# Performance work log

Hardware: AMD Instinct MI355X
Metric: run time of the kernel (lower is better)

Reference implementation:

```python
import jax, jax.numpy as jnp
import numpy as np

TARGET_RADIUS = 0.99
EPS = 1e-8


def _effective_W_h(W_h):
    """Spectral-norm constraint: 3 power iterations (no grad through u,v),
    then rescale W_h so its spectral radius is TARGET_RADIUS."""
    dim = W_h.shape[0]
    u = jax.random.normal(jax.random.key(1), (dim,), dtype=W_h.dtype)
    u = u / jnp.linalg.norm(u)
    Ws = jax.lax.stop_gradient(W_h)
    v = None
    for _ in range(3):
        v = Ws.T @ u
        v = v / (jnp.linalg.norm(v) + EPS)
        u = Ws @ v
        u = u / (jnp.linalg.norm(u) + EPS)
    sigma = jnp.abs(u @ W_h @ v)  # grad flows only through W_h here
    return W_h * (TARGET_RADIUS / (sigma + EPS))


def setup_inputs() -> dict:
    key = jax.random.key(0)
    ks = jax.random.split(key, 6)
    T, B, D = 2048, 16, 1024
    xavier = float(np.sqrt(6.0 / (D + D)))
    return {
        "x": jax.random.normal(ks[0], (T, B, D), dtype=jnp.float32),
        "h0": jnp.zeros((B, D), dtype=jnp.float32),
        "W_x": jax.random.uniform(ks[1], (D, D), jnp.float32, -xavier, xavier),
        "W_h": jax.random.uniform(ks[2], (D, D), jnp.float32, -xavier, xavier),
        "W_delta": jax.random.uniform(ks[3], (D, D), jnp.float32, -0.1 * xavier, 0.1 * xavier),
        "b": jnp.zeros((D,), dtype=jnp.float32),
        "b_delta": jnp.full((D,), -2.0, dtype=jnp.float32),
        "b_gate": jnp.zeros((D,), dtype=jnp.float32),
    }


def reference(x, h0, W_x, W_h, W_delta, b, b_delta, b_gate):
    # x: [T, B, D]; h0: [B, D]
    W_h_eff = _effective_W_h(W_h)
    # Batch the input-side GEMMs over all timesteps at once.
    delta_raw = jnp.einsum("tbd,ed->tbe", x, W_delta) + b_delta  # [T,B,D]
    cand_x = jnp.einsum("tbd,ed->tbe", x, W_x) + b               # [T,B,D]

    def step(h_prev, inputs):
        x_t, dr_t, cx_t = inputs
        delta = jax.nn.sigmoid(dr_t)
        candidate = jnp.tanh(cx_t + h_prev @ W_h_eff.T)
        h_new = (1.0 - delta) * h_prev + delta * candidate
        out_t = h_new * jax.nn.silu(h_new + x_t + b_gate)
        return h_new, (out_t, h_new)

    _, (output, hs) = jax.lax.scan(step, h0, (x, delta_raw, cand_x))
    h = jnp.concatenate([h0[None], hs], axis=0)  # [T+1, B, D]
    return output, h
```

## Files before the change

kernel.cpp:

```cpp
#include <hip/hip_runtime.h>
#include <hip/hip_fp16.h>
#include <stdint.h>

#define TT 2048
#define BB 16
#define DD 1024
static const size_t H0OFF = 33554432;

typedef _Float16 f16;
typedef _Float16 f16x2 __attribute__((ext_vector_type(2)));
typedef _Float16 f16x8 __attribute__((ext_vector_type(8)));
typedef float f32x4 __attribute__((ext_vector_type(4)));

__device__ __forceinline__ float erfinv_xla(float x) {
  float w = -log1pf(-x * x);
  float p;
  if (w < 5.0f) {
    w -= 2.5f;
    p = 2.81022636e-08f;
    p = fmaf(p, w, 3.43273939e-07f);
    p = fmaf(p, w, -3.5233877e-06f);
    p = fmaf(p, w, -4.39150654e-06f);
    p = fmaf(p, w, 0.00021858087f);
    p = fmaf(p, w, -0.00125372503f);
    p = fmaf(p, w, -0.00417768164f);
    p = fmaf(p, w, 0.246640727f);
    p = fmaf(p, w, 1.50140941f);
  } else {
    w = sqrtf(w) - 3.0f;
    p = -0.000200214257f;
    p = fmaf(p, w, 0.000100950558f);
    p = fmaf(p, w, 0.00134934322f);
    p = fmaf(p, w, -0.00367342844f);
    p = fmaf(p, w, 0.00573950773f);
    p = fmaf(p, w, -0.0076224613f);
    p = fmaf(p, w, 0.00943887047f);
    p = fmaf(p, w, 1.00167406f);
    p = fmaf(p, w, 2.83297682f);
  }
  return p * x;
}

__device__ __forceinline__ float bits_to_normal(unsigned bits) {
  unsigned fb = (bits >> 9) | 0x3f800000u;
  float f = __uint_as_float(fb) - 1.0f;
  const float lo = -0.99999994f;
  float u = f * 2.0f + lo;
  u = fmaxf(lo, u);
  return __uint_as_float(0x3fb504f3u) * erfinv_xla(u);
}

#define TF_ROUND(r) { x0 += x1; x1 = (x1 << r) | (x1 >> (32 - r)); x1 ^= x0; }

__global__ void k_u0(float* t0, float* u) {
  __shared__ float red[512];
  int i = threadIdx.x;
  unsigned ks0 = 0u, ks1 = 1u, ks2 = 0x1BD11BDAu ^ 0u ^ 1u;
  unsigned x0 = (unsigned)i + ks0;
  unsigned x1 = (unsigned)(i + 512) + ks1;
  TF_ROUND(13) TF_ROUND(15) TF_ROUND(26) TF_ROUND(6)
  x0 += ks1; x1 += ks2 + 1u;
  TF_ROUND(17) TF_ROUND(29) TF_ROUND(16) TF_ROUND(24)
  x0 += ks2; x1 += ks0 + 2u;
  TF_ROUND(13) TF_ROUND(15) TF_ROUND(26) TF_ROUND(6)
  x0 += ks0; x1 += ks1 + 3u;
  TF_ROUND(17) TF_ROUND(29) TF_ROUND(16) TF_ROUND(24)
  x0 += ks1; x1 += ks2 + 4u;
  TF_ROUND(13) TF_ROUND(15) TF_ROUND(26) TF_ROUND(6)
  x0 += ks2; x1 += ks0 + 5u;
  float z0 = bits_to_normal(x0);
  float z1 = bits_to_normal(x1);
  t0[i] = z0; t0[i + 512] = z1;
  red[i] = z0 * z0 + z1 * z1;
  __syncthreads();
  for (int s = 256; s > 0; s >>= 1) { if (i < s) red[i] += red[i + s]; __syncthreads(); }
  float inv = 1.0f / sqrtf(red[0]);
  u[i] = t0[i] * inv; u[i + 512] = t0[i + 512] * inv;
}

__global__ void k_mvT(const float* __restrict__ W, const float* __restrict__ u,
                      float* __restrict__ out) {
  int j = blockIdx.x * 256 + threadIdx.x;
  float acc = 0.f;
  for (int i = 0; i < DD; ++i) acc = fmaf(W[(size_t)i * DD + j], u[i], acc);
  out[j] = acc;
}

__global__ void k_mv(const float* __restrict__ W, const float* __restrict__ v,
                     float* __restrict__ out) {
  int gtid = blockIdx.x * 256 + threadIdx.x;
  int wave = gtid >> 6, lane = threadIdx.x & 63;
  for (int rr = 0; rr < 16; ++rr) {
    int row = wave * 16 + rr;
    float acc = 0.f;
    for (int c = 0; c < 16; ++c) {
      int col = c * 64 + lane;
      acc = fmaf(W[(size_t)row * DD + col], v[col], acc);
    }
    for (int off = 32; off > 0; off >>= 1) acc += __shfl_down(acc, off, 64);
    if (lane == 0) out[row] = acc;
  }
}

__global__ void k_norm(const float* __restrict__ src, float* __restrict__ dst, float eps) {
  __shared__ float red[1024];
  int i = threadIdx.x;
  float xv = src[i];
  red[i] = xv * xv;
  __syncthreads();
  for (int s = 512; s > 0; s >>= 1) { if (i < s) red[i] += red[i + s]; __syncthreads(); }
  float inv = 1.0f / (sqrtf(red[0]) + eps);
  dst[i] = src[i] * inv;
}

__global__ void k_sigma(const float* __restrict__ u, const float* __restrict__ wv,
                        float* __restrict__ scale) {
  __shared__ float red[1024];
  int i = threadIdx.x;
  red[i] = u[i] * wv[i];
  __syncthreads();
  for (int s = 512; s > 0; s >>= 1) { if (i < s) red[i] += red[i + s]; __syncthreads(); }
  if (i == 0) scale[0] = 0.99f / (fabsf(red[0]) + 1e-8f);
}

__global__ void k_castWh(const float* __restrict__ Wh, const float* __restrict__ scale,
                         f16* __restrict__ WhH) {
  int i = blockIdx.x * 256 + threadIdx.x;
  float s = scale[0];
  WhH[i] = (f16)(Wh[i] * s);
}

__global__ __launch_bounds__(256) void k_gemm(const float* __restrict__ X,
                                              const float* __restrict__ Wt,
                                              const float* __restrict__ bias,
                                              float* __restrict__ Cout) {
  __shared__ __align__(16) f16 Ah[128 * 64];
  __shared__ __align__(16) f16 Bh[128 * 64];
  int m0 = blockIdx.x * 128, n0 = blockIdx.y * 128;
  int tid = threadIdx.x, lane = tid & 63, w = tid >> 6;
  int wm = w & 1, wn = w >> 1;
  int srow = tid >> 3, scol = (tid & 7) * 8;
  f32x4 acc[4][4];
#pragma unroll
  for (int i = 0; i < 4; ++i)
#pragma unroll
    for (int j = 0; j < 4; ++j) acc[i][j] = (f32x4){0.f, 0.f, 0.f, 0.f};

  for (int kt = 0; kt < 16; ++kt) {
    int k0 = kt * 64;
#pragma unroll
    for (int c = 0; c < 4; ++c) {
      int row = c * 32 + srow;
      const float4* sa = (const float4*)(X + (size_t)(m0 + row) * DD + k0 + scol);
      float4 a0 = sa[0], a1 = sa[1];
      f16x8 hv;
      hv[0] = (f16)a0.x; hv[1] = (f16)a0.y; hv[2] = (f16)a0.z; hv[3] = (f16)a0.w;
      hv[4] = (f16)a1.x; hv[5] = (f16)a1.y; hv[6] = (f16)a1.z; hv[7] = (f16)a1.w;
      *(f16x8*)&Ah[row * 64 + scol] = hv;
      const float4* sb = (const float4*)(Wt + (size_t)(n0 + row) * DD + k0 + scol);
      float4 b0 = sb[0], b1 = sb[1];
      f16x8 hw;
      hw[0] = (f16)b0.x; hw[1] = (f16)b0.y; hw[2] = (f16)b0.z; hw[3] = (f16)b0.w;
      hw[4] = (f16)b1.x; hw[5] = (f16)b1.y; hw[6] = (f16)b1.z; hw[7] = (f16)b1.w;
      *(f16x8*)&Bh[row * 64 + scol] = hw;
    }
    __syncthreads();
#pragma unroll
    for (int ks = 0; ks < 2; ++ks) {
      f16x8 af[4], bf[4];
#pragma unroll
      for (int i = 0; i < 4; ++i)
        af[i] = *(const f16x8*)&Ah[(wm * 64 + i * 16 + (lane & 15)) * 64 + ks * 32 + (lane >> 4) * 8];
#pragma unroll
      for (int j = 0; j < 4; ++j)
        bf[j] = *(const f16x8*)&Bh[(wn * 64 + j * 16 + (lane & 15)) * 64 + ks * 32 + (lane >> 4) * 8];
#pragma unroll
      for (int i = 0; i < 4; ++i)
#pragma unroll
        for (int j = 0; j < 4; ++j)
          acc[i][j] = __builtin_amdgcn_mfma_f32_16x16x32_f16(af[i], bf[j], acc[i][j], 0, 0, 0);
    }
    __syncthreads();
  }
#pragma unroll
  for (int j = 0; j < 4; ++j) {
    int col = n0 + wn * 64 + j * 16 + (lane & 15);
    float bs = bias[col];
#pragma unroll
    for (int i = 0; i < 4; ++i) {
      int rbase = m0 + wm * 64 + i * 16 + (lane >> 4) * 4;
#pragma unroll
      for (int r = 0; r < 4; ++r)
        Cout[(size_t)(rbase + r) * DD + col] = acc[i][j][r] + bs;
    }
  }
}

__device__ __forceinline__ float fdot2u(uint32_t a, uint32_t b, float c) {
#if __has_builtin(__builtin_amdgcn_fdot2)
  return __builtin_amdgcn_fdot2(__builtin_bit_cast(f16x2, a),
                                __builtin_bit_cast(f16x2, b), c, false);
#else
  f16x2 av = __builtin_bit_cast(f16x2, a), bv = __builtin_bit_cast(f16x2, b);
  return c + (float)av[0] * (float)bv[0] + (float)av[1] * (float)bv[1];
#endif
}

__device__ __forceinline__ float sigmoid_fast(float v) {
  return 1.0f / (1.0f + __expf(-v));
}
__device__ __forceinline__ float tanh_fast(float v) {
  float t = __expf(-2.0f * fabsf(v));
  float r = (1.0f - t) / (1.0f + t);
  return copysignf(r, v);
}

__global__ __launch_bounds__(256, 1) void k_rec(const float* __restrict__ x,
                                                const float* __restrict__ h0,
                                                const float* __restrict__ b_gate,
                                                const f16* __restrict__ WhH,
                                                uint32_t* __restrict__ hx,
                                                float* __restrict__ d_out) {
  int bid = blockIdx.x;
  int batch = bid & 15;
  int eslice = bid >> 4;
  int tid = threadIdx.x, lane = tid & 63, wv = tid >> 6;

  __shared__ uint32_t WT[512 * 64];
  __shared__ __align__(16) uint16_t hsh[1024];
  __shared__ float partial[4][64];

  {
    int r = tid >> 2, q = tid & 3;
    const uint32_t* src = (const uint32_t*)(WhH + (size_t)(64 * eslice + r) * DD) + q * 128;
#pragma unroll 8
    for (int j = 0; j < 128; ++j)
      WT[(q * 128 + j) * 64 + r] = src[j];
  }
  {
    const float* hb = h0 + (size_t)batch * DD + 4 * tid;
    float a0 = hb[0], a1 = hb[1], a2 = hb[2], a3 = hb[3];
    uint32_t lo = ((uint32_t)__builtin_bit_cast(uint16_t, (f16)a0)) |
                  ((uint32_t)__builtin_bit_cast(uint16_t, (f16)a1) << 16);
    uint32_t hi = ((uint32_t)__builtin_bit_cast(uint16_t, (f16)a2)) |
                  ((uint32_t)__builtin_bit_cast(uint16_t, (f16)a3) << 16);
    uint2 pk; pk.x = lo; pk.y = hi;
    ((uint2*)hsh)[tid] = pk;
  }

  float h_own = 0.f, bgv = 0.f, cx_c = 0.f, dr_c = 0.f, xv_c = 0.f;
  int e_g = 64 * eslice + lane;
  if (wv == 0) {
    size_t b0 = (size_t)batch * DD + e_g;
    h_own = h0[b0];
    bgv = b_gate[e_g];
    d_out[H0OFF + b0] = h_own;
    cx_c = d_out[b0];
    dr_c = d_out[H0OFF + 16384 + b0];
    xv_c = x[b0];
  }
  __syncthreads();

  const uint4* hq4 = (const uint4*)hsh;

#pragma unroll 1
  for (int t = 0; t < TT; ++t) {
    float cx_n = 0.f, dr_n = 0.f, xv_n = 0.f;
    if (wv == 0 && t + 1 < TT) {
      size_t bn = (size_t)(t + 1) * 16384 + (size_t)batch * DD + e_g;
      cx_n = d_out[bn];
      dr_n = d_out[H0OFF + 16384 + bn];
      xv_n = x[bn];
    }

    float a0 = 0.f, a1 = 0.f, a2 = 0.f, a3 = 0.f;
#pragma unroll
    for (int k = 0; k < 32; ++k) {
      uint4 hh = hq4[32 * wv + k];
      int d4 = 128 * wv + 4 * k;
      a0 = fdot2u(WT[(d4 + 0) * 64 + lane], hh.x, a0);
      a1 = fdot2u(WT[(d4 + 1) * 64 + lane], hh.y, a1);
      a2 = fdot2u(WT[(d4 + 2) * 64 + lane], hh.z, a2);
      a3 = fdot2u(WT[(d4 + 3) * 64 + lane], hh.w, a3);
    }
    partial[wv][lane] = (a0 + a1) + (a2 + a3);
    __syncthreads();

    uint32_t want = (uint32_t)(t + 1);
    uint32_t* slot = hx + (size_t)(want & 15u) * (BB * DD) + (size_t)batch * DD;

    if (wv == 0) {
      float hdot = (partial[0][lane] + partial[1][lane]) +
                   (partial[2][lane] + partial[3][lane]);
      float dlt = sigmoid_fast(dr_c);
      float cand = tanh_fast(cx_c + hdot);
      float hn = fmaf(dlt, cand - h_own, h_own);
      uint16_t hb = __builtin_bit_cast(uint16_t, (f16)hn);
      __hip_atomic_store(&slot[e_g], (want << 16) | (uint32_t)hb,
                         __ATOMIC_RELAXED, __HIP_MEMORY_SCOPE_AGENT);
      size_t base = (size_t)t * 16384 + (size_t)batch * DD + e_g;
      float z = hn + xv_c + bgv;
      d_out[base] = hn * z * sigmoid_fast(z);
      d_out[H0OFF + 16384 + base] = hn;
      h_own = hn; cx_c = cx_n; dr_c = dr_n; xv_c = xv_n;
    }

    if (t + 1 < TT) {
      uint32_t* wp = slot + 4 * tid;
      uint32_t w0, w1, w2, w3;
      while (true) {
        w0 = __hip_atomic_load(wp + 0, __ATOMIC_RELAXED, __HIP_MEMORY_SCOPE_AGENT);
        w1 = __hip_atomic_load(wp + 1, __ATOMIC_RELAXED, __HIP_MEMORY_SCOPE_AGENT);
        w2 = __hip_atomic_load(wp + 2, __ATOMIC_RELAXED, __HIP_MEMORY_SCOPE_AGENT);
        w3 = __hip_atomic_load(wp + 3, __ATOMIC_RELAXED, __HIP_MEMORY_SCOPE_AGENT);
        bool ok = ((w0 >> 16) == want) & ((w1 >> 16) == want) &
                  ((w2 >> 16) == want) & ((w3 >> 16) == want);
        if (__all(ok)) break;
      }
      uint2 pk;
      pk.x = (w0 & 0xffffu) | (w1 << 16);
      pk.y = (w2 & 0xffffu) | (w3 << 16);
      ((uint2*)hsh)[tid] = pk;
      __syncthreads();
    }
  }
}

extern "C" void kernel_launch(void* const* d_in, const int* in_sizes, int n_in,
                              void* d_out_v, int out_size, void* d_ws, size_t ws_size,
                              hipStream_t stream) {
  const float* x  = (const float*)d_in[0];
  const float* h0 = (const float*)d_in[1];
  const float* Wx = (const float*)d_in[2];
  const float* Wh = (const float*)d_in[3];
  const float* Wd = (const float*)d_in[4];
  const float* b  = (const float*)d_in[5];
  const float* bd = (const float*)d_in[6];
  const float* bg = (const float*)d_in[7];
  float* out = (float*)d_out_v;

  char* ws = (char*)d_ws;
  float* u    = (float*)(ws + 0);
  float* v    = (float*)(ws + 4096);
  float* t0   = (float*)(ws + 8192);
  float* sc   = (float*)(ws + 12288);
  uint32_t* hx = (uint32_t*)(ws + 65536);
  f16* WhH  = (f16*)(ws + 2097152);

  hipMemsetAsync(hx, 0, (size_t)16 * BB * DD * 4, stream);

  k_u0<<<1, 512, 0, stream>>>(t0, u);
  for (int it = 0; it < 3; ++it) {
    k_mvT<<<4, 256, 0, stream>>>(Wh, u, t0);
    k_norm<<<1, 1024, 0, stream>>>(t0, v, 1e-8f);
    k_mv<<<16, 256, 0, stream>>>(Wh, v, t0);
    k_norm<<<1, 1024, 0, stream>>>(t0, u, 1e-8f);
  }
  k_sigma<<<1, 1024, 0, stream>>>(u, t0, sc);
  k_castWh<<<4096, 256, 0, stream>>>(Wh, sc, WhH);

  dim3 gg(256, 8, 1);
  k_gemm<<<gg, 256, 0, stream>>>(x, Wx, b, out);
  k_gemm<<<gg, 256, 0, stream>>>(x, Wd, bd, out + H0OFF + 16384);

  k_rec<<<256, 256, 0, stream>>>(x, h0, bg, WhH, hx, out);
}
```

Before: 5.038 ms.

## Keep W_h slice in registers, double-buffer partials, dual-path flag polling

The recurrence kernel now runs 512 threads per block and holds each thread's slice of the fp16 W_h in 64 VGPRs, replacing the LDS-resident transposed copy. The partial-sum buffer is double-buffered by step parity, and the cross-block wait moves to the top of each step so there is one barrier per step instead of two. Each tagged h value is published to two mirror buffers: one is polled with sc0 loads that skip the L1, the other is read with agent-scope atomics every fourth spin. The intent is to cut LDS traffic and handoff latency on the serial critical path. The cost is heavy register pressure, inline asm, and reliance on cache-coherence behaviour of the sc0 path.

```diff
diff --git a/kernel.cpp b/kernel.cpp
--- a/kernel.cpp
+++ b/kernel.cpp
@@ -11,6 +11,8 @@
 typedef _Float16 f16x2 __attribute__((ext_vector_type(2)));
 typedef _Float16 f16x8 __attribute__((ext_vector_type(8)));
 typedef float f32x4 __attribute__((ext_vector_type(4)));
+typedef unsigned u32x2 __attribute__((ext_vector_type(2)));
+typedef unsigned u32x4 __attribute__((ext_vector_type(4)));
 
 __device__ __forceinline__ float erfinv_xla(float x) {
   float w = -log1pf(-x * x);
@@ -215,42 +217,49 @@
   return copysignf(r, v);
 }
 
-__global__ __launch_bounds__(256, 1) void k_rec(const float* __restrict__ x,
+__device__ __forceinline__ u32x2 load2_sc0(const uint32_t* p) {
+  u32x2 v;
+  asm volatile("global_load_dwordx2 %0, %1, off sc0\n\ts_waitcnt vmcnt(0)"
+               : "=v"(v) : "v"(p) : "memory");
+  return v;
+}
+
+__global__ __launch_bounds__(512, 1) void k_rec(const float* __restrict__ x,
                                                 const float* __restrict__ h0,
                                                 const float* __restrict__ b_gate,
                                                 const f16* __restrict__ WhH,
-                                                uint32_t* __restrict__ hx,
+                                                uint32_t* __restrict__ hxF,
+                                                uint32_t* __restrict__ hxS,
                                                 float* __restrict__ d_out) {
   int bid = blockIdx.x;
   int batch = bid & 15;
   int eslice = bid >> 4;
   int tid = threadIdx.x, lane = tid & 63, wv = tid >> 6;
 
-  __shared__ uint32_t WT[512 * 64];
   __shared__ __align__(16) uint16_t hsh[1024];
-  __shared__ float partial[4][64];
+  __shared__ float partial[2][8][64];
+
+  const u32x4* wp = (const u32x4*)(WhH + (size_t)(64 * eslice + lane) * DD + 128 * wv);
+  u32x4 w0 = wp[0],  w1 = wp[1],  w2 = wp[2],  w3 = wp[3];
+  u32x4 w4 = wp[4],  w5 = wp[5],  w6 = wp[6],  w7 = wp[7];
+  u32x4 w8 = wp[8],  w9 = wp[9],  w10 = wp[10], w11 = wp[11];
+  u32x4 w12 = wp[12], w13 = wp[13], w14 = wp[14], w15 = wp[15];
+  asm volatile("" : "+v"(w0), "+v"(w1), "+v"(w2), "+v"(w3));
+  asm volatile("" : "+v"(w4), "+v"(w5), "+v"(w6), "+v"(w7));
+  asm volatile("" : "+v"(w8), "+v"(w9), "+v"(w10), "+v"(w11));
+  asm volatile("" : "+v"(w12), "+v"(w13), "+v"(w14), "+v"(w15));
 
   {
-    int r = tid >> 2, q = tid & 3;
-    const uint32_t* src = (const uint32_t*)(WhH + (size_t)(64 * eslice + r) * DD) + q * 128;
-#pragma unroll 8
-    for (int j = 0; j < 128; ++j)
-      WT[(q * 128 + j) * 64 + r] = src[j];
-  }
-  {
-    const float* hb = h0 + (size_t)batch * DD + 4 * tid;
-    float a0 = hb[0], a1 = hb[1], a2 = hb[2], a3 = hb[3];
-    uint32_t lo = ((uint32_t)__builtin_bit_cast(uint16_t, (f16)a0)) |
-                  ((uint32_t)__builtin_bit_cast(uint16_t, (f16)a1) << 16);
-    uint32_t hi = ((uint32_t)__builtin_bit_cast(uint16_t, (f16)a2)) |
-                  ((uint32_t)__builtin_bit_cast(uint16_t, (f16)a3) << 16);
-    uint2 pk; pk.x = lo; pk.y = hi;
-    ((uint2*)hsh)[tid] = pk;
+    float2 hv = *(const float2*)(h0 + (size_t)batch * DD + 2 * tid);
+    uint32_t pk = ((uint32_t)__builtin_bit_cast(uint16_t, (f16)hv.x)) |
+                  ((uint32_t)__builtin_bit_cast(uint16_t, (f16)hv.y) << 16);
+    ((uint32_t*)hsh)[tid] = pk;
   }
 
   float h_own = 0.f, bgv = 0.f, cx_c = 0.f, dr_c = 0.f, xv_c = 0.f;
   int e_g = 64 * eslice + lane;
   if (wv == 0) {
+    __builtin_amdgcn_s_setprio(1);
     size_t b0 = (size_t)batch * DD + e_g;
     h_own = h0[b0];
     bgv = b_gate[e_g];
@@ -261,10 +270,34 @@
   }
   __syncthreads();
 
-  const uint4* hq4 = (const uint4*)hsh;
+  const u32x4* hq4 = (const u32x4*)hsh;
 
 #pragma unroll 1
   for (int t = 0; t < TT; ++t) {
+    if (t > 0) {
+      uint32_t want = (uint32_t)t;
+      size_t soff = (size_t)(want & 15u) * (BB * DD) + (size_t)batch * DD + 2 * tid;
+      const uint32_t* fp = hxF + soff;
+      const uint32_t* sp = hxS + soff;
+      uint32_t a0w, a1w;
+      int it = 0;
+      while (true) {
+        if ((it & 3) == 3) {
+          uint64_t q = __hip_atomic_load((const uint64_t*)sp, __ATOMIC_RELAXED,
+                                         __HIP_MEMORY_SCOPE_AGENT);
+          a0w = (uint32_t)q; a1w = (uint32_t)(q >> 32);
+        } else {
+          u32x2 q = load2_sc0(fp);
+          a0w = q[0]; a1w = q[1];
+        }
+        bool ok = ((a0w >> 16) == want) & ((a1w >> 16) == want);
+        if (__all(ok)) break;
+        ++it;
+      }
+      ((uint32_t*)hsh)[tid] = (a0w & 0xffffu) | (a1w << 16);
+      asm volatile("s_waitcnt lgkmcnt(0)" ::: "memory");
+    }
+
     float cx_n = 0.f, dr_n = 0.f, xv_n = 0.f;
     if (wv == 0 && t + 1 < TT) {
       size_t bn = (size_t)(t + 1) * 16384 + (size_t)batch * DD + e_g;
@@ -273,55 +306,48 @@
       xv_n = x[bn];
     }
 
-    float a0 = 0.f, a1 = 0.f, a2 = 0.f, a3 = 0.f;
-#pragma unroll
-    for (int k = 0; k < 32; ++k) {
-      uint4 hh = hq4[32 * wv + k];
-      int d4 = 128 * wv + 4 * k;
-      a0 = fdot2u(WT[(d4 + 0) * 64 + lane], hh.x, a0);
-      a1 = fdot2u(WT[(d4 + 1) * 64 + lane], hh.y, a1);
-      a2 = fdot2u(WT[(d4 + 2) * 64 + lane], hh.z, a2);
-      a3 = fdot2u(WT[(d4 + 3) * 64 + lane], hh.w, a3);
-    }
-    partial[wv][lane] = (a0 + a1) + (a2 + a3);
+    {
+      float a0 = 0.f, a1 = 0.f, a2 = 0.f, a3 = 0.f;
+      u32x4 hh;
+      hh = hq4[16 * wv + 0];  a0 = fdot2u(w0[0], hh[0], a0);  a0 = fdot2u(w0[1], hh[1], a0);  a0 = fdot2u(w0[2], hh[2], a0);  a0 = fdot2u(w0[3], hh[3], a0);
+      hh = hq4[16 * wv + 1];  a1 = fdot2u(w1[0], hh[0], a1);  a1 = fdot2u(w1[1], hh[1], a1);  a1 = fdot2u(w1[2], hh[2], a1);  a1 = fdot2u(w1[3], hh[3], a1);
+      hh = hq4[16 * wv + 2];  a2 = fdot2u(w2[0], hh[0], a2);  a2 = fdot2u(w2[1], hh[1], a2);  a2 = fdot2u(w2[2], hh[2], a2);  a2 = fdot2u(w2[3], hh[3], a2);
+      hh = hq4[16 * wv + 3];  a3 = fdot2u(w3[0], hh[0], a3);  a3 = fdot2u(w3[1], hh[1], a3);  a3 = fdot2u(w3[2], hh[2], a3);  a3 = fdot2u(w3[3], hh[3], a3);
+      hh = hq4[16 * wv + 4];  a0 = fdot2u(w4[0], hh[0], a0);  a0 = fdot2u(w4[1], hh[1], a0);  a0 = fdot2u(w4[2], hh[2], a0);  a0 = fdot2u(w4[3], hh[3], a0);
+      hh = hq4[16 * wv + 5];  a1 = fdot2u(w5[0], hh[0], a1);  a1 = fdot2u(w5[1], hh[1], a1);  a1 = fdot2u(w5[2], hh[2], a1);  a1 = fdot2u(w5[3], hh[3], a1);
+      hh = hq4[16 * wv + 6];  a2 = fdot2u(w6[0], hh[0], a2);  a2 = fdot2u(w6[1], hh[1], a2);  a2 = fdot2u(w6[2], hh[2], a2);  a2 = fdot2u(w6[3], hh[3], a2);
+      hh = hq4[16 * wv + 7];  a3 = fdot2u(w7[0], hh[0], a3);  a3 = fdot2u(w7[1], hh[1], a3);  a3 = fdot2u(w7[2], hh[2], a3);  a3 = fdot2u(w7[3], hh[3], a3);
+      hh = hq4[16 * wv + 8];  a0 = fdot2u(w8[0], hh[0], a0);  a0 = fdot2u(w8[1], hh[1], a0);  a0 = fdot2u(w8[2], hh[2], a0);  a0 = fdot2u(w8[3], hh[3], a0);
+      hh = hq4[16 * wv + 9];  a1 = fdot2u(w9[0], hh[0], a1);  a1 = fdot2u(w9[1], hh[1], a1);  a1 = fdot2u(w9[2], hh[2], a1);  a1 = fdot2u(w9[3], hh[3], a1);
+      hh = hq4[16 * wv + 10]; a2 = fdot2u(w10[0], hh[0], a2); a2 = fdot2u(w10[1], hh[1], a2); a2 = fdot2u(w10[2], hh[2], a2); a2 = fdot2u(w10[3], hh[3], a2);
+      hh = hq4[16 * wv + 11]; a3 = fdot2u(w11[0], hh[0], a3); a3 = fdot2u(w11[1], hh[1], a3); a3 = fdot2u(w11[2], hh[2], a3); a3 = fdot2u(w11[3], hh[3], a3);
+      hh = hq4[16 * wv + 12]; a0 = fdot2u(w12[0], hh[0], a0); a0 = fdot2u(w12[1], hh[1], a0); a0 = fdot2u(w12[2], hh[2], a0); a0 = fdot2u(w12[3], hh[3], a0);
+      hh = hq4[16 * wv + 13]; a1 = fdot2u(w13[0], hh[0], a1); a1 = fdot2u(w13[1], hh[1], a1); a1 = fdot2u(w13[2], hh[2], a1); a1 = fdot2u(w13[3], hh[3], a1);
+      hh = hq4[16 * wv + 14]; a2 = fdot2u(w14[0], hh[0], a2); a2 = fdot2u(w14[1], hh[1], a2); a2 = fdot2u(w14[2], hh[2], a2); a2 = fdot2u(w14[3], hh[3], a2);
+      hh = hq4[16 * wv + 15]; a3 = fdot2u(w15[0], hh[0], a3); a3 = fdot2u(w15[1], hh[1], a3); a3 = fdot2u(w15[2], hh[2], a3); a3 = fdot2u(w15[3], hh[3], a3);
+      partial[t & 1][wv][lane] = (a0 + a1) + (a2 + a3);
+    }
     __syncthreads();
 
-    uint32_t want = (uint32_t)(t + 1);
-    uint32_t* slot = hx + (size_t)(want & 15u) * (BB * DD) + (size_t)batch * DD;
-
     if (wv == 0) {
-      float hdot = (partial[0][lane] + partial[1][lane]) +
-                   (partial[2][lane] + partial[3][lane]);
+      const float* pp = &partial[t & 1][0][lane];
+      float hdot = ((pp[0] + pp[64]) + (pp[128] + pp[192])) +
+                   ((pp[256] + pp[320]) + (pp[384] + pp[448]));
       float dlt = sigmoid_fast(dr_c);
       float cand = tanh_fast(cx_c + hdot);
       float hn = fmaf(dlt, cand - h_own, h_own);
+      uint32_t want1 = (uint32_t)(t + 1);
       uint16_t hb = __builtin_bit_cast(uint16_t, (f16)hn);
-      __hip_atomic_store(&slot[e_g], (want << 16) | (uint32_t)hb,
-                         __ATOMIC_RELAXED, __HIP_MEMORY_SCOPE_AGENT);
+      uint32_t tagged = (want1 << 16) | (uint32_t)hb;
+      size_t poff = (size_t)(want1 & 15u) * (BB * DD) + (size_t)batch * DD + e_g;
+      *(volatile uint32_t*)(hxF + poff) = tagged;
+      __hip_atomic_store(hxS + poff, tagged, __ATOMIC_RELAXED,
+                         __HIP_MEMORY_SCOPE_AGENT);
       size_t base = (size_t)t * 16384 + (size_t)batch * DD + e_g;
       float z = hn + xv_c + bgv;
       d_out[base] = hn * z * sigmoid_fast(z);
       d_out[H0OFF + 16384 + base] = hn;
       h_own = hn; cx_c = cx_n; dr_c = dr_n; xv_c = xv_n;
-    }
-
-    if (t + 1 < TT) {
-      uint32_t* wp = slot + 4 * tid;
-      uint32_t w0, w1, w2, w3;
-      while (true) {
-        w0 = __hip_atomic_load(wp + 0, __ATOMIC_RELAXED, __HIP_MEMORY_SCOPE_AGENT);
-        w1 = __hip_atomic_load(wp + 1, __ATOMIC_RELAXED, __HIP_MEMORY_SCOPE_AGENT);
-        w2 = __hip_atomic_load(wp + 2, __ATOMIC_RELAXED, __HIP_MEMORY_SCOPE_AGENT);
-        w3 = __hip_atomic_load(wp + 3, __ATOMIC_RELAXED, __HIP_MEMORY_SCOPE_AGENT);
-        bool ok = ((w0 >> 16) == want) & ((w1 >> 16) == want) &
-                  ((w2 >> 16) == want) & ((w3 >> 16) == want);
-        if (__all(ok)) break;
-      }
-      uint2 pk;
-      pk.x = (w0 & 0xffffu) | (w1 << 16);
-      pk.y = (w2 & 0xffffu) | (w3 << 16);
-      ((uint2*)hsh)[tid] = pk;
-      __syncthreads();
     }
   }
 }
@@ -344,10 +370,12 @@
   float* v    = (float*)(ws + 4096);
   float* t0   = (float*)(ws + 8192);
   float* sc   = (float*)(ws + 12288);
-  uint32_t* hx = (uint32_t*)(ws + 65536);
-  f16* WhH  = (f16*)(ws + 2097152);
-
-  hipMemsetAsync(hx, 0, (size_t)16 * BB * DD * 4, stream);
+  uint32_t* hxF = (uint32_t*)(ws + 65536);
+  uint32_t* hxS = (uint32_t*)(ws + 1114112);
+  f16* WhH  = (f16*)(ws + 4194304);
+
+  (void)hipMemsetAsync(hxF, 0, (size_t)16 * BB * DD * 4, stream);
+  (void)hipMemsetAsync(hxS, 0, (size_t)16 * BB * DD * 4, stream);
 
   k_u0<<<1, 512, 0, stream>>>(t0, u);
   for (int it = 0; it < 3; ++it) {
@@ -363,5 +391,5 @@
   k_gemm<<<gg, 256, 0, stream>>>(x, Wx, b, out);
   k_gemm<<<gg, 256, 0, stream>>>(x, Wd, bd, out + H0OFF + 16384);
 
-  k_rec<<<256, 256, 0, stream>>>(x, h0, bg, WhH, hx, out);
-}
+  k_rec<<<256, 512, 0, stream>>>(x, h0, bg, WhH, hxF, hxS, out);
+}
```

After: 4.848 ms. 3.8% less time.

## Split recurrent matvec over input dims, keep weights in registers, exchange partial sums

Applied to the files above, without the earlier changes.

Each block previously owned 64 output rows of W_h in LDS and had to gather the full new h vector from all blocks every step. Now each block owns a 64-wide input-column slice of W_h, held in VGPRs across 512 threads, and computes f16 partial dot products for all 1024 outputs using only its own locally produced h slice. It publishes those partials through a 4-deep tagged ring in global memory, and wave 0 polls and sums the 16 partials for its own outputs. This removes LDS weight reads and the full-h broadcast. In exchange, it adds more polled words per lane and rounds the partial sums to f16, which costs precision. A leftover duplicate dot-product loop whose results are discarded may add compute unless the compiler removes it.

```diff
diff --git a/kernel.cpp b/kernel.cpp
--- a/kernel.cpp
+++ b/kernel.cpp
@@ -7,10 +7,15 @@
 #define DD 1024
 static const size_t H0OFF = 33554432;
 
+#define PSTRIDE 1040
+#define PB (16 * PSTRIDE)
+#define SLOTW (16 * PB)
+
 typedef _Float16 f16;
 typedef _Float16 f16x2 __attribute__((ext_vector_type(2)));
 typedef _Float16 f16x8 __attribute__((ext_vector_type(8)));
 typedef float f32x4 __attribute__((ext_vector_type(4)));
+typedef unsigned u32x4 __attribute__((ext_vector_type(4)));
 
 __device__ __forceinline__ float erfinv_xla(float x) {
   float w = -log1pf(-x * x);
@@ -215,7 +220,14 @@
   return copysignf(r, v);
 }
 
-__global__ __launch_bounds__(256, 1) void k_rec(const float* __restrict__ x,
+__device__ __forceinline__ uint32_t f16bits(float v) {
+  return (uint32_t)__builtin_bit_cast(uint16_t, (f16)v);
+}
+__device__ __forceinline__ float f16val(uint32_t w) {
+  return (float)__builtin_bit_cast(f16, (uint16_t)(w & 0xffffu));
+}
+
+__global__ __launch_bounds__(512, 1) void k_rec(const float* __restrict__ x,
                                                 const float* __restrict__ h0,
                                                 const float* __restrict__ b_gate,
                                                 const f16* __restrict__ WhH,
@@ -226,31 +238,25 @@
   int eslice = bid >> 4;
   int tid = threadIdx.x, lane = tid & 63, wv = tid >> 6;
 
-  __shared__ uint32_t WT[512 * 64];
-  __shared__ __align__(16) uint16_t hsh[1024];
-  __shared__ float partial[4][64];
-
+  __shared__ uint32_t hls[2][32];
+
+  int e1 = 128 * wv + lane, e2 = e1 + 64;
+  u32x4 wA[8], wB[8];
   {
-    int r = tid >> 2, q = tid & 3;
-    const uint32_t* src = (const uint32_t*)(WhH + (size_t)(64 * eslice + r) * DD) + q * 128;
-#pragma unroll 8
-    for (int j = 0; j < 128; ++j)
-      WT[(q * 128 + j) * 64 + r] = src[j];
-  }
-  {
-    const float* hb = h0 + (size_t)batch * DD + 4 * tid;
-    float a0 = hb[0], a1 = hb[1], a2 = hb[2], a3 = hb[3];
-    uint32_t lo = ((uint32_t)__builtin_bit_cast(uint16_t, (f16)a0)) |
-                  ((uint32_t)__builtin_bit_cast(uint16_t, (f16)a1) << 16);
-    uint32_t hi = ((uint32_t)__builtin_bit_cast(uint16_t, (f16)a2)) |
-                  ((uint32_t)__builtin_bit_cast(uint16_t, (f16)a3) << 16);
-    uint2 pk; pk.x = lo; pk.y = hi;
-    ((uint2*)hsh)[tid] = pk;
-  }
+    const u32x4* p1 = (const u32x4*)(WhH + (size_t)e1 * DD + 64 * eslice);
+    const u32x4* p2 = (const u32x4*)(WhH + (size_t)e2 * DD + 64 * eslice);
+#pragma unroll
+    for (int j = 0; j < 8; ++j) { wA[j] = p1[j]; wB[j] = p2[j]; }
+  }
+  asm volatile("" : "+v"(wA[0]), "+v"(wA[1]), "+v"(wA[2]), "+v"(wA[3]));
+  asm volatile("" : "+v"(wA[4]), "+v"(wA[5]), "+v"(wA[6]), "+v"(wA[7]));
+  asm volatile("" : "+v"(wB[0]), "+v"(wB[1]), "+v"(wB[2]), "+v"(wB[3]));
+  asm volatile("" : "+v"(wB[4]), "+v"(wB[5]), "+v"(wB[6]), "+v"(wB[7]));
 
   float h_own = 0.f, bgv = 0.f, cx_c = 0.f, dr_c = 0.f, xv_c = 0.f;
   int e_g = 64 * eslice + lane;
   if (wv == 0) {
+    __builtin_amdgcn_s_setprio(1);
     size_t b0 = (size_t)batch * DD + e_g;
     h_own = h0[b0];
     bgv = b_gate[e_g];
@@ -258,71 +264,94 @@
     cx_c = d_out[b0];
     dr_c = d_out[H0OFF + 16384 + b0];
     xv_c = x[b0];
+    float v0 = __shfl(h_own, 2 * (lane & 31), 64);
+    float v1 = __shfl(h_own, 2 * (lane & 31) + 1, 64);
+    if (lane < 32)
+      hls[0][lane] = f16bits(v0) | (f16bits(v1) << 16);
   }
   __syncthreads();
 
-  const uint4* hq4 = (const uint4*)hsh;
+  size_t pubrow = (size_t)batch * PB + (size_t)eslice * PSTRIDE;
+  const uint32_t* pollbase = hx + (size_t)batch * PB + e_g;
 
 #pragma unroll 1
   for (int t = 0; t < TT; ++t) {
-    float cx_n = 0.f, dr_n = 0.f, xv_n = 0.f;
-    if (wv == 0 && t + 1 < TT) {
-      size_t bn = (size_t)(t + 1) * 16384 + (size_t)batch * DD + e_g;
-      cx_n = d_out[bn];
-      dr_n = d_out[H0OFF + 16384 + bn];
-      xv_n = x[bn];
-    }
-
-    float a0 = 0.f, a1 = 0.f, a2 = 0.f, a3 = 0.f;
-#pragma unroll
-    for (int k = 0; k < 32; ++k) {
-      uint4 hh = hq4[32 * wv + k];
-      int d4 = 128 * wv + 4 * k;
-      a0 = fdot2u(WT[(d4 + 0) * 64 + lane], hh.x, a0);
-      a1 = fdot2u(WT[(d4 + 1) * 64 + lane], hh.y, a1);
-      a2 = fdot2u(WT[(d4 + 2) * 64 + lane], hh.z, a2);
-      a3 = fdot2u(WT[(d4 + 3) * 64 + lane], hh.w, a3);
-    }
-    partial[wv][lane] = (a0 + a1) + (a2 + a3);
-    __syncthreads();
-
-    uint32_t want = (uint32_t)(t + 1);
-    uint32_t* slot = hx + (size_t)(want & 15u) * (BB * DD) + (size_t)batch * DD;
+    uint32_t tag = (uint32_t)(t + 1);
+    {
+      const u32x4* hl4 = (const u32x4*)&hls[t & 1][0];
+      float a0 = 0.f, a1 = 0.f, b0 = 0.f, b1 = 0.f;
+#pragma unroll
+      for (int j = 0; j < 4; ++j) {
+        u32x4 hh = hl4[j];
+        a0 = fdot2u(wA[2 * j][0], hh[0], a0);     a0 = fdot2u(wA[2 * j][1], hh[1], a0);
+        a0 = fdot2u(wA[2 * j][2], hh[2], a0);     a0 = fdot2u(wA[2 * j][3], hh[3], a0);
+        b0 = fdot2u(wB[2 * j][0], hh[0], b0);     b0 = fdot2u(wB[2 * j][1], hh[1], b0);
+        b0 = fdot2u(wB[2 * j][2], hh[2], b0);     b0 = fdot2u(wB[2 * j][3], hh[3], b0);
+        u32x4 hg = hl4[j + 4];
+        a1 = fdot2u(wA[2 * j + 1][0], hg[0], a1); a1 = fdot2u(wA[2 * j + 1][1], hg[1], a1);
+        a1 = fdot2u(wA[2 * j + 1][2], hg[2], a1); a1 = fdot2u(wA[2 * j + 1][3], hg[3], a1);
+        b1 = fdot2u(wB[2 * j + 1][0], hg[0], b1); b1 = fdot2u(wB[2 * j + 1][1], hg[1], b1);
+        b1 = fdot2u(wB[2 * j + 1][2], hg[2], b1); b1 = fdot2u(wB[2 * j + 1][3], hg[3], b1);
+      }
+      a0 = 0.f; a1 = 0.f; b0 = 0.f; b1 = 0.f;
+#pragma unroll
+      for (int k = 0; k < 8; ++k) {
+        u32x4 hh = hl4[k];
+        float aa = (k & 1) ? a1 : a0;
+        float bb = (k & 1) ? b1 : b0;
+        aa = fdot2u(wA[k][0], hh[0], aa); aa = fdot2u(wA[k][1], hh[1], aa);
+        aa = fdot2u(wA[k][2], hh[2], aa); aa = fdot2u(wA[k][3], hh[3], aa);
+        bb = fdot2u(wB[k][0], hh[0], bb); bb = fdot2u(wB[k][1], hh[1], bb);
+        bb = fdot2u(wB[k][2], hh[2], bb); bb = fdot2u(wB[k][3], hh[3], bb);
+        if (k & 1) { a1 = aa; b1 = bb; } else { a0 = aa; b0 = bb; }
+      }
+      float pa = a0 + a1, pb = b0 + b1;
+      uint32_t* pub = hx + (size_t)(tag & 3u) * SLOTW + pubrow;
+      __hip_atomic_store(pub + e1, (tag << 16) | f16bits(pa),
+                         __ATOMIC_RELAXED, __HIP_MEMORY_SCOPE_AGENT);
+      __hip_atomic_store(pub + e2, (tag << 16) | f16bits(pb),
+                         __ATOMIC_RELAXED, __HIP_MEMORY_SCOPE_AGENT);
+    }
 
     if (wv == 0) {
-      float hdot = (partial[0][lane] + partial[1][lane]) +
-                   (partial[2][lane] + partial[3][lane]);
+      float cx_n = 0.f, dr_n = 0.f, xv_n = 0.f;
+      if (t + 1 < TT) {
+        size_t bn = (size_t)(t + 1) * 16384 + (size_t)batch * DD + e_g;
+        cx_n = d_out[bn];
+        dr_n = d_out[H0OFF + 16384 + bn];
+        xv_n = x[bn];
+      }
+      const uint32_t* pp = pollbase + (size_t)(tag & 3u) * SLOTW;
+      uint32_t v[16];
+      bool ok;
+      do {
+        ok = true;
+#pragma unroll
+        for (int p = 0; p < 16; ++p)
+          v[p] = __hip_atomic_load(pp + p * PSTRIDE, __ATOMIC_RELAXED,
+                                   __HIP_MEMORY_SCOPE_AGENT);
+#pragma unroll
+        for (int p = 0; p < 16; ++p) ok &= ((v[p] >> 16) == tag);
+      } while (!__all(ok));
+      float s0 = (f16val(v[0]) + f16val(v[1])) + (f16val(v[2]) + f16val(v[3]));
+      float s1 = (f16val(v[4]) + f16val(v[5])) + (f16val(v[6]) + f16val(v[7]));
+      float s2 = (f16val(v[8]) + f16val(v[9])) + (f16val(v[10]) + f16val(v[11]));
+      float s3 = (f16val(v[12]) + f16val(v[13])) + (f16val(v[14]) + f16val(v[15]));
+      float hdot = (s0 + s1) + (s2 + s3);
       float dlt = sigmoid_fast(dr_c);
       float cand = tanh_fast(cx_c + hdot);
       float hn = fmaf(dlt, cand - h_own, h_own);
-      uint16_t hb = __builtin_bit_cast(uint16_t, (f16)hn);
-      __hip_atomic_store(&slot[e_g], (want << 16) | (uint32_t)hb,
-                         __ATOMIC_RELAXED, __HIP_MEMORY_SCOPE_AGENT);
       size_t base = (size_t)t * 16384 + (size_t)batch * DD + e_g;
       float z = hn + xv_c + bgv;
       d_out[base] = hn * z * sigmoid_fast(z);
       d_out[H0OFF + 16384 + base] = hn;
+      float v0 = __shfl(hn, 2 * (lane & 31), 64);
+      float v1 = __shfl(hn, 2 * (lane & 31) + 1, 64);
+      if (t + 1 < TT && lane < 32)
+        hls[(t + 1) & 1][lane] = f16bits(v0) | (f16bits(v1) << 16);
       h_own = hn; cx_c = cx_n; dr_c = dr_n; xv_c = xv_n;
     }
-
-    if (t + 1 < TT) {
-      uint32_t* wp = slot + 4 * tid;
-      uint32_t w0, w1, w2, w3;
-      while (true) {
-        w0 = __hip_atomic_load(wp + 0, __ATOMIC_RELAXED, __HIP_MEMORY_SCOPE_AGENT);
-        w1 = __hip_atomic_load(wp + 1, __ATOMIC_RELAXED, __HIP_MEMORY_SCOPE_AGENT);
-        w2 = __hip_atomic_load(wp + 2, __ATOMIC_RELAXED, __HIP_MEMORY_SCOPE_AGENT);
-        w3 = __hip_atomic_load(wp + 3, __ATOMIC_RELAXED, __HIP_MEMORY_SCOPE_AGENT);
-        bool ok = ((w0 >> 16) == want) & ((w1 >> 16) == want) &
-                  ((w2 >> 16) == want) & ((w3 >> 16) == want);
-        if (__all(ok)) break;
-      }
-      uint2 pk;
-      pk.x = (w0 & 0xffffu) | (w1 << 16);
-      pk.y = (w2 & 0xffffu) | (w3 << 16);
-      ((uint2*)hsh)[tid] = pk;
-      __syncthreads();
-    }
+    __syncthreads();
   }
 }
 
@@ -344,10 +373,10 @@
   float* v    = (float*)(ws + 4096);
   float* t0   = (float*)(ws + 8192);
   float* sc   = (float*)(ws + 12288);
-  uint32_t* hx = (uint32_t*)(ws + 65536);
-  f16* WhH  = (f16*)(ws + 2097152);
-
-  hipMemsetAsync(hx, 0, (size_t)16 * BB * DD * 4, stream);
+  uint32_t* hx = (uint32_t*)(ws + 16384);
+  f16* WhH  = (f16*)(ws + 4280320);
+
+  (void)hipMemsetAsync(hx, 0, (size_t)4 * SLOTW * 4, stream);
 
   k_u0<<<1, 512, 0, stream>>>(t0, u);
   for (int it = 0; it < 3; ++it) {
@@ -363,5 +392,5 @@
   k_gemm<<<gg, 256, 0, stream>>>(x, Wx, b, out);
   k_gemm<<<gg, 256, 0, stream>>>(x, Wd, bd, out + H0OFF + 16384);
 
-  k_rec<<<256, 256, 0, stream>>>(x, h0, bg, WhH, hx, out);
-}
+  k_rec<<<256, 512, 0, stream>>>(x, h0, bg, WhH, hx, out);
+}
```

Result: faster. 4.912 ms (-2.5%).
